# Performance work log

Hardware: AMD Instinct MI355X
Metric: run time of the kernel (lower is better)

The kernel has to match this reference:

```python
import jax, jax.numpy as jnp
import numpy as np

NMS_THRESHOLD = 0.4
TOP_K = 1000
MAX_BOXES = 300
N_ANCHORS = 300000
N_CLASSES = 80
DET_DIM = 85


def setup_inputs() -> dict:
    key = jax.random.key(0)
    k1, k2, k3, k4 = jax.random.split(key, 4)
    # valid [y1, x1, y2, x2] boxes: top-left corner + positive height/width
    yx = jax.random.uniform(k1, (1, N_ANCHORS, 2), jnp.float32) * 512.0
    hw = jax.random.uniform(k2, (1, N_ANCHORS, 2), jnp.float32) * 64.0 + 1.0
    boxes = jnp.concatenate([yx, yx + hw], axis=-1)
    classification = jax.random.uniform(k3, (1, N_ANCHORS, N_CLASSES), jnp.float32)
    detections = jax.random.normal(k4, (1, N_ANCHORS, DET_DIM), jnp.float32)
    return {"boxes": boxes, "classification": classification, "detections": detections}


def _iou_matrix(b):
    # b: [K, 4] as [y1, x1, y2, x2]
    y1, x1, y2, x2 = b[:, 0], b[:, 1], b[:, 2], b[:, 3]
    area = (y2 - y1) * (x2 - x1)
    ih = jnp.clip(jnp.minimum(y2[:, None], y2[None, :]) - jnp.maximum(y1[:, None], y1[None, :]), 0.0)
    iw = jnp.clip(jnp.minimum(x2[:, None], x2[None, :]) - jnp.maximum(x1[:, None], x1[None, :]), 0.0)
    inter = ih * iw
    return inter / (area[:, None] + area[None, :] - inter + 1e-8)


def _nms_forward(boxes, classification, detections):
    b = boxes[0]                      # [N, 4]
    cls = classification[0]           # [N, C]
    det = detections[0]               # [N, D]
    scores = jnp.max(cls, axis=1)     # [N]
    # pre-NMS top-k filter (lax.top_k returns scores sorted descending)
    _, idx = jax.lax.top_k(scores, TOP_K)
    b_k = b[idx]                      # [K, 4]
    det_k = det[idx]                  # [K, D]
    iou = _iou_matrix(b_k)            # [K, K]
    # greedy NMS over score-sorted candidates: keep box i iff no higher-scoring
    # kept box overlaps it above the threshold
    def step(keep, i):
        suppressed = jnp.any(keep & (iou[i] > NMS_THRESHOLD))
        return keep.at[i].set(~suppressed), None
    keep, _ = jax.lax.scan(step, jnp.zeros(TOP_K, dtype=bool), jnp.arange(TOP_K))
    # first MAX_BOXES kept candidates (in score order), zero-padded
    pos = jnp.where(keep, jnp.arange(TOP_K), TOP_K)
    pos = jnp.sort(pos)[:MAX_BOXES]
    valid = pos < TOP_K
    sel = det_k[jnp.minimum(pos, TOP_K - 1)]          # [MAX_BOXES, D]
    out = jnp.where(valid[:, None], sel, 0.0)
    return out[None]                   # [1, MAX_BOXES, D]


def reference(boxes, classification, detections):
    return _nms_forward(boxes, classification, detections)
```

## Files before the change

kernel.cpp:

```cpp
#include <hip/hip_runtime.h>
#include <stdint.h>

typedef unsigned long long u64;

#define N_ANCH   300000
#define N_CLS    80
#define DET_DIM  85
#define TOPK     1000
#define MAXB     300
#define NMS_THR  0.4f
#define CAP      4096
#define N4       (N_ANCH / 4)

#define NB_HIST  80
#define NB_RANK  96
#define NB_MASK  250

#define OFF_SBITS   0
#define OFF_HA      300032
#define OFF_HB      304128
#define OFF_META    308224
#define OFF_CAND    308288
#define OFF_TOPK    316480
#define OFF_BOXK    317480
#define OFF_MASK    321480

__global__ __launch_bounds__(256) void k_scores(const float4* __restrict__ cls4,
                                                uint32_t* __restrict__ sbits,
                                                uint32_t* __restrict__ ha,
                                                uint32_t* __restrict__ hb,
                                                uint32_t* __restrict__ meta) {
    int tid = threadIdx.x;
    if (blockIdx.x == 0) {
        if (tid == 0) meta[4] = 0;
        for (int i = tid; i < 4096; i += 256) { ha[i] = 0; hb[i] = 0; }
    }
    int wave = tid >> 6, lane = tid & 63, g = lane >> 2, q = lane & 3;
    int row = blockIdx.x * 64 + wave * 16 + g;
    if (row >= N_ANCH) return;
    const float4* rp = cls4 + (size_t)row * 20;
    float m = -1.0f;
    #pragma unroll
    for (int k = 0; k < 5; k++) {
        float4 v = rp[q + k * 4];
        m = fmaxf(m, fmaxf(fmaxf(v.x, v.y), fmaxf(v.z, v.w)));
    }
    m = fmaxf(m, __shfl_xor(m, 1));
    m = fmaxf(m, __shfl_xor(m, 2));
    if (q == 0) sbits[row] = __float_as_uint(m);
}

__device__ __forceinline__ void agg_add(uint32_t* h, uint32_t bin, bool valid) {
    int lane = threadIdx.x & 63;
    bool done = !valid;
    while (true) {
        unsigned long long rem = __ballot(!done);
        if (rem == 0ull) break;
        int leader = __ffsll((long long)rem) - 1;
        uint32_t lbin = __shfl(bin, leader);
        bool mine = (!done) && (bin == lbin);
        unsigned long long grp = __ballot(mine);
        if (lane == leader) atomicAdd(&h[lbin], (uint32_t)__popcll(grp));
        done = done || mine;
    }
}

__device__ __forceinline__ void findthr_core(const uint32_t c[4], uint32_t* wred,
                                             uint32_t K, uint32_t* res) {
    int tid = threadIdx.x, lane = tid & 63, wave = tid >> 6;
    uint32_t s = c[0] + c[1] + c[2] + c[3];
    uint32_t x = s;
    #pragma unroll
    for (int off = 1; off < 64; off <<= 1) {
        uint32_t v = __shfl_up(x, off);
        if (lane >= off) x += v;
    }
    if (lane == 63) wred[wave] = x;
    __syncthreads();
    if (wave == 0) {
        uint32_t w = (lane < 16) ? wred[lane] : 0u;
        #pragma unroll
        for (int off = 1; off < 16; off <<= 1) {
            uint32_t v = __shfl_up(w, off);
            if (lane >= off) w += v;
        }
        if (lane < 16) wred[lane] = w;
    }
    __syncthreads();
    uint32_t base = (wave == 0) ? 0u : wred[wave - 1];
    uint32_t incl = base + x, excl = incl - s;
    if (excl < K && incl >= K) {
        uint32_t run = excl;
        #pragma unroll
        for (int k = 0; k < 4; k++) {
            uint32_t nr = run + c[k];
            if (run < K && nr >= K) { res[0] = 4095 - (tid * 4 + k); res[1] = run; }
            run = nr;
        }
    }
    __syncthreads();
}

__device__ __forceinline__ void load_bins(const uint32_t* __restrict__ hist, uint32_t c[4]) {
    uint4 q = ((const uint4*)hist)[1023 - threadIdx.x];
    c[0] = q.w; c[1] = q.z; c[2] = q.y; c[3] = q.x;
}

__global__ __launch_bounds__(1024) void k_histA(const uint4* __restrict__ sb4,
                                                uint32_t* __restrict__ ha) {
    __shared__ uint32_t h[4096];
    int tid = threadIdx.x;
    for (int i = tid; i < 4096; i += 1024) h[i] = 0;
    __syncthreads();
    int t4 = blockIdx.x * 1024 + tid;
    bool v = t4 < N4;
    uint4 sv = v ? sb4[t4] : make_uint4(0, 0, 0, 0);
    agg_add(h, sv.x >> 20, v);
    agg_add(h, sv.y >> 20, v);
    agg_add(h, sv.z >> 20, v);
    agg_add(h, sv.w >> 20, v);
    __syncthreads();
    for (int i = tid; i < 4096; i += 1024) { uint32_t c = h[i]; if (c) atomicAdd(&ha[i], c); }
}

__global__ __launch_bounds__(1024) void k_histB(const uint4* __restrict__ sb4,
                                                const uint32_t* __restrict__ ha,
                                                uint32_t* __restrict__ hb) {
    __shared__ uint32_t h[4096];
    __shared__ uint32_t wred[16];
    __shared__ uint32_t mr[2];
    int tid = threadIdx.x;
    uint32_t c[4];
    load_bins(ha, c);
    findthr_core(c, wred, TOPK, mr);
    uint32_t binA = mr[0];
    for (int i = tid; i < 4096; i += 1024) h[i] = 0;
    __syncthreads();
    int t4 = blockIdx.x * 1024 + tid;
    if (t4 < N4) {
        uint4 sv = sb4[t4];
        if ((sv.x >> 20) == binA) atomicAdd(&h[(sv.x >> 8) & 0xFFFu], 1u);
        if ((sv.y >> 20) == binA) atomicAdd(&h[(sv.y >> 8) & 0xFFFu], 1u);
        if ((sv.z >> 20) == binA) atomicAdd(&h[(sv.z >> 8) & 0xFFFu], 1u);
        if ((sv.w >> 20) == binA) atomicAdd(&h[(sv.w >> 8) & 0xFFFu], 1u);
    }
    __syncthreads();
    for (int i = tid; i < 4096; i += 1024) { uint32_t v = h[i]; if (v) atomicAdd(&hb[i], v); }
}

__global__ __launch_bounds__(1024) void k_compact(const uint4* __restrict__ sb4,
                                                  const uint32_t* __restrict__ ha,
                                                  const uint32_t* __restrict__ hb,
                                                  uint32_t* __restrict__ meta,
                                                  u64* __restrict__ cand) {
    __shared__ uint32_t wred[16];
    __shared__ uint32_t mr[2];
    int tid = threadIdx.x, lane = tid & 63;
    uint32_t c[4];
    load_bins(ha, c);
    findthr_core(c, wred, TOPK, mr);
    uint32_t binA = mr[0], GA = mr[1];
    load_bins(hb, c);
    findthr_core(c, wred, TOPK - GA, mr);
    uint32_t T24 = (binA << 12) | mr[0];
    int t4 = blockIdx.x * 1024 + tid;
    bool v = t4 < N4;
    uint4 sv = v ? sb4[t4] : make_uint4(0, 0, 0, 0);
    uint32_t sl[4] = {sv.x, sv.y, sv.z, sv.w};
    #pragma unroll
    for (int s = 0; s < 4; s++) {
        uint32_t sb = sl[s];
        bool m = v && ((sb >> 8) >= T24);
        unsigned long long b = __ballot(m);
        if (b) {
            int leader = __ffsll((long long)b) - 1;
            uint32_t base2 = 0;
            if (lane == leader) base2 = atomicAdd(&meta[4], (uint32_t)__popcll(b));
            base2 = __shfl(base2, leader);
            if (m) {
                uint32_t p = base2 + (uint32_t)__popcll(b & ((1ull << lane) - 1ull));
                uint32_t idx = (uint32_t)(t4 * 4 + s);
                if (p < CAP) cand[p] = ((u64)sb << 32) | (uint32_t)(~idx);
            }
        }
    }
}

__global__ __launch_bounds__(1024) void k_rank(const u64* __restrict__ cand,
                                               const uint32_t* __restrict__ meta,
                                               uint32_t* __restrict__ topk,
                                               const float4* __restrict__ boxes4,
                                               float4* __restrict__ boxk) {
    __shared__ u64 candS[CAP];
    int tid = threadIdx.x, wave = tid >> 6, lane = tid & 63;
    uint32_t C = meta[4]; if (C > CAP) C = CAP;
    uint32_t Cpad = (C + 63u) & ~63u;
    for (uint32_t t = tid; t < Cpad; t += 1024) candS[t] = (t < C) ? cand[t] : 0ull;
    __syncthreads();
    for (uint32_t i = (uint32_t)(blockIdx.x * 16 + wave); i < C; i += NB_RANK * 16) {
        u64 my = candS[i];
        uint32_t r = 0;
        for (uint32_t j0 = 0; j0 < Cpad; j0 += 64)
            r += (uint32_t)__popcll(__ballot(candS[j0 + lane] > my));
        if (r < TOPK && lane == 0) {
            uint32_t idx = ~(uint32_t)(my & 0xFFFFFFFFull);
            if (idx < N_ANCH) { topk[r] = idx; boxk[r] = boxes4[idx]; }
        }
    }
}

__global__ __launch_bounds__(1024) void k_mask(const float4* __restrict__ boxk,
                                               u64* __restrict__ M) {
    __shared__ float4 bks[TOPK];
    __shared__ float areaS[TOPK];
    int tid = threadIdx.x, wave = tid >> 6, lane = tid & 63;
    for (int i = tid; i < TOPK; i += 1024) {
        float4 b = boxk[i];
        bks[i] = b;
        {
            #pragma clang fp contract(off)
            areaS[i] = (b.z - b.x) * (b.w - b.y);
        }
    }
    __syncthreads();
    for (int gw = blockIdx.x * 16 + wave; gw < TOPK * 16; gw += NB_MASK * 16) {
        int i = gw >> 4, w = gw & 15;
        int j = w * 64 + lane, jc = j < TOPK ? j : 0;
        float4 bi = bks[i], bj = bks[jc];
        bool ok;
        {
            #pragma clang fp contract(off)
            float ih = fminf(bi.z, bj.z) - fmaxf(bi.x, bj.x); ih = fmaxf(ih, 0.0f);
            float iw = fminf(bi.w, bj.w) - fmaxf(bi.y, bj.y); iw = fmaxf(iw, 0.0f);
            float inter = ih * iw;
            float denom = (areaS[i] + areaS[jc] - inter) + 1e-8f;
            ok = (j < TOPK) && (inter / denom > NMS_THR);
        }
        unsigned long long m = __ballot(ok);
        if (lane == 0) M[i * 16 + w] = m;
    }
}

#define MSW(i, w) ((i) * 16 + (((w) + (i)) & 15))

__global__ __launch_bounds__(1024) void k_scan(const u64* __restrict__ M,
                                               const uint32_t* __restrict__ topk,
                                               const float* __restrict__ det,
                                               float* __restrict__ out) {
    __shared__ __align__(16) u64 MS[16000];
    __shared__ int keeplS[MAXB];
    int tid = threadIdx.x, lane = tid & 63;
    for (int t = tid; t < TOPK * 16; t += 1024) {
        int i = t >> 4, w = t & 15;
        MS[MSW(i, w)] = M[t];
    }
    __syncthreads();
    if (tid < 64) {
        u64 keptArr[16];
        #pragma unroll
        for (int cc = 0; cc < 16; cc++) {
            int i = cc * 64 + lane;
            u64 pre = 0ull, Mic = 0ull;
            if (i < TOPK) {
                #pragma unroll
                for (int w = 0; w < cc; w++) pre |= MS[MSW(i, w)] & keptArr[w];
                Mic = MS[MSW(i, cc)];
            }
            unsigned long long pre_mask = __ballot(pre != 0ull);
            u64 kc = 0ull;
            const int lim = (cc == 15) ? (TOPK - 960) : 64;
            for (int k = 0; k < lim; k++) {
                unsigned long long b = __ballot(((Mic >> k) & 1ull) != 0ull);
                bool sup = (((pre_mask >> k) & 1ull) != 0ull) || ((b & kc) != 0ull);
                kc |= sup ? 0ull : (1ull << k);
            }
            keptArr[cc] = kc;
        }
        uint32_t pfxw[16];
        uint32_t run = 0;
        #pragma unroll
        for (int w = 0; w < 16; w++) { pfxw[w] = run; run += (uint32_t)__popcll(keptArr[w]); }
        int total = (int)run; if (total > MAXB) total = MAXB;
        for (int r = total + lane; r < MAXB; r += 64) keeplS[r] = -1;
        #pragma unroll
        for (int w = 0; w < 16; w++) {
            int i = w * 64 + lane;
            if (i < TOPK) {
                u64 kw = keptArr[w];
                if ((kw >> lane) & 1ull) {
                    uint32_t rank = pfxw[w] + (uint32_t)__popcll(kw & ((1ull << lane) - 1ull));
                    if (rank < MAXB) keeplS[rank] = i;
                }
            }
        }
    }
    __syncthreads();
    for (int t = tid; t < MAXB * DET_DIM; t += 1024) {
        int r = t / DET_DIM, col = t - r * DET_DIM;
        int pos = keeplS[r];
        float v = 0.0f;
        if (pos >= 0) {
            uint32_t src = topk[pos];
            if (src < N_ANCH) v = det[(size_t)src * DET_DIM + col];
        }
        out[t] = v;
    }
}

extern "C" void kernel_launch(void* const* d_in, const int* in_sizes, int n_in,
                              void* d_out, int out_size, void* d_ws, size_t ws_size,
                              hipStream_t stream) {
    const float4* boxes4 = (const float4*)d_in[0];
    const float4* cls4   = (const float4*)d_in[1];
    const float*  det    = (const float*)d_in[2];
    float* out = (float*)d_out;
    uint32_t* ws = (uint32_t*)d_ws;

    uint32_t* sbits = ws + OFF_SBITS;
    uint32_t* ha    = ws + OFF_HA;
    uint32_t* hb    = ws + OFF_HB;
    uint32_t* meta  = ws + OFF_META;
    u64*      cand  = (u64*)(ws + OFF_CAND);
    uint32_t* topk  = ws + OFF_TOPK;
    float4*   boxk  = (float4*)(ws + OFF_BOXK);
    u64*      M     = (u64*)(ws + OFF_MASK);

    k_scores <<<(N_ANCH + 63) / 64, 256, 0, stream>>>(cls4, sbits, ha, hb, meta);
    k_histA  <<<NB_HIST, 1024, 0, stream>>>((const uint4*)sbits, ha);
    k_histB  <<<NB_HIST, 1024, 0, stream>>>((const uint4*)sbits, ha, hb);
    k_compact<<<NB_HIST, 1024, 0, stream>>>((const uint4*)sbits, ha, hb, meta, cand);
    k_rank   <<<NB_RANK, 1024, 0, stream>>>(cand, meta, topk, boxes4, boxk);
    k_mask   <<<NB_MASK, 1024, 0, stream>>>(boxk, M);
    k_scan   <<<1, 1024, 0, stream>>>(M, topk, det, out);
}
```

Measured before the change: 280.0 us.

## Replace serial greedy NMS scan with parallel fixed-point iteration across block

The single-wave sequential greedy NMS over 1000 candidates is replaced by a block-wide iteration. Starting from everything kept, each of the 1024 threads re-evaluates whether its candidate is suppressed by currently kept higher-scoring boxes, and the loop stops when the keep set no longer changes. Each thread also reads its own mask row straight into registers, so the LDS staging of the whole mask matrix goes away. The iteration count depends on how long suppression chains are in the data. Each iteration costs two block barriers.

```diff
diff --git a/kernel.cpp b/kernel.cpp
--- a/kernel.cpp
+++ b/kernel.cpp
@@ -241,58 +241,57 @@
     }
 }
 
-#define MSW(i, w) ((i) * 16 + (((w) + (i)) & 15))
-
 __global__ __launch_bounds__(1024) void k_scan(const u64* __restrict__ M,
                                                const uint32_t* __restrict__ topk,
                                                const float* __restrict__ det,
                                                float* __restrict__ out) {
-    __shared__ __align__(16) u64 MS[16000];
+    __shared__ u64 kbufA[16], kbufB[16];
+    __shared__ uint32_t chgF[16];
     __shared__ int keeplS[MAXB];
-    int tid = threadIdx.x, lane = tid & 63;
-    for (int t = tid; t < TOPK * 16; t += 1024) {
-        int i = t >> 4, w = t & 15;
-        MS[MSW(i, w)] = M[t];
-    }
-    __syncthreads();
-    if (tid < 64) {
-        u64 keptArr[16];
+    const int tid = threadIdx.x, wave = tid >> 6, lane = tid & 63;
+    const bool vr = tid < TOPK;
+
+    u64 Mpre[16];
+    #pragma unroll
+    for (int w = 0; w < 16; w++) {
+        u64 row = vr ? M[(size_t)tid * 16 + w] : 0ull;
+        u64 pm = (w < wave) ? ~0ull : ((w == wave) ? ((1ull << lane) - 1ull) : 0ull);
+        Mpre[w] = row & pm;
+    }
+    if (tid < 15) kbufA[tid] = ~0ull;
+    if (tid == 15) kbufA[15] = (1ull << (TOPK - 960)) - 1ull;
+    __syncthreads();
+
+    u64* cur = kbufA;
+    u64* nxt = kbufB;
+    for (int it = 0; it < TOPK + 2; ++it) {
+        u64 sup = 0ull;
         #pragma unroll
-        for (int cc = 0; cc < 16; cc++) {
-            int i = cc * 64 + lane;
-            u64 pre = 0ull, Mic = 0ull;
-            if (i < TOPK) {
-                #pragma unroll
-                for (int w = 0; w < cc; w++) pre |= MS[MSW(i, w)] & keptArr[w];
-                Mic = MS[MSW(i, cc)];
-            }
-            unsigned long long pre_mask = __ballot(pre != 0ull);
-            u64 kc = 0ull;
-            const int lim = (cc == 15) ? (TOPK - 960) : 64;
-            for (int k = 0; k < lim; k++) {
-                unsigned long long b = __ballot(((Mic >> k) & 1ull) != 0ull);
-                bool sup = (((pre_mask >> k) & 1ull) != 0ull) || ((b & kc) != 0ull);
-                kc |= sup ? 0ull : (1ull << k);
-            }
-            keptArr[cc] = kc;
-        }
-        uint32_t pfxw[16];
-        uint32_t run = 0;
+        for (int w = 0; w < 16; w++) sup |= Mpre[w] & cur[w];
+        bool nk = vr && (sup == 0ull);
+        u64 bal = __ballot(nk);
+        if (lane == 0) { nxt[wave] = bal; chgF[wave] = (bal != cur[wave]) ? 1u : 0u; }
+        __syncthreads();
+        uint32_t any = 0;
         #pragma unroll
-        for (int w = 0; w < 16; w++) { pfxw[w] = run; run += (uint32_t)__popcll(keptArr[w]); }
-        int total = (int)run; if (total > MAXB) total = MAXB;
-        for (int r = total + lane; r < MAXB; r += 64) keeplS[r] = -1;
-        #pragma unroll
-        for (int w = 0; w < 16; w++) {
-            int i = w * 64 + lane;
-            if (i < TOPK) {
-                u64 kw = keptArr[w];
-                if ((kw >> lane) & 1ull) {
-                    uint32_t rank = pfxw[w] + (uint32_t)__popcll(kw & ((1ull << lane) - 1ull));
-                    if (rank < MAXB) keeplS[rank] = i;
-                }
-            }
-        }
+        for (int w = 0; w < 16; w++) any |= chgF[w];
+        __syncthreads();
+        u64* t = cur; cur = nxt; nxt = t;
+        if (!any) break;
+    }
+
+    u64 kw = cur[wave];
+    uint32_t pfx = 0;
+    #pragma unroll
+    for (int w = 0; w < 16; w++) {
+        uint32_t p = (uint32_t)__popcll(cur[w]);
+        if (w < wave) pfx += p;
+    }
+    if (tid < MAXB) keeplS[tid] = -1;
+    __syncthreads();
+    if (vr && ((kw >> lane) & 1ull)) {
+        uint32_t rank = pfx + (uint32_t)__popcll(kw & ((1ull << lane) - 1ull));
+        if (rank < MAXB) keeplS[rank] = tid;
     }
     __syncthreads();
     for (int t = tid; t < MAXB * DET_DIM; t += 1024) {
```

Measured after the change: 255.6 us. 8.7% less time.
